# Performance work log

Hardware: AMD Instinct MI355X
Metric: run time of the kernel (lower is better)

The kernel has to match this reference:

```python
import jax, jax.numpy as jnp
import numpy as np

B, T, V, E, H = 4096, 80, 80, 8, 256  # batch, seq_len, num_classes/vocab, embed dim, n_hidden
FORGET_BIAS = 1.0  # tf BasicLSTMCell default


def lstm_layer(x, W, b):
    """Run one BasicLSTMCell layer over time. x: [B, T, D]; W: [D+H, 4H]; b: [4H].
    TF BasicLSTMCell gate order is (i, j, f, o); new_c = c*sig(f+fb) + sig(i)*tanh(j)."""
    Bsz = x.shape[0]

    def step(carry, xt):
        c, h = carry
        gates = jnp.concatenate([xt, h], axis=-1) @ W + b  # [B, 4H]
        i, j, f, o = jnp.split(gates, 4, axis=-1)
        c = c * jax.nn.sigmoid(f + FORGET_BIAS) + jax.nn.sigmoid(i) * jnp.tanh(j)
        h = jnp.tanh(c) * jax.nn.sigmoid(o)
        return (c, h), h

    init = (jnp.zeros((Bsz, H), x.dtype), jnp.zeros((Bsz, H), x.dtype))
    _, hs = jax.lax.scan(step, init, jnp.swapaxes(x, 0, 1))  # hs: [T, B, H]
    return jnp.swapaxes(hs, 0, 1)  # [B, T, H]


def setup_inputs() -> dict:
    key = jax.random.key(0)
    ks = jax.random.split(key, 8)
    features = jax.random.randint(ks[0], (B, T), 0, V, dtype=jnp.int32)
    labels = jax.random.randint(ks[1], (B,), 0, V, dtype=jnp.int32)
    emb = jax.random.normal(ks[2], (V, E), dtype=jnp.float32) * 0.1  # trainable=False in original
    W1 = jax.random.normal(ks[3], (E + H, 4 * H), dtype=jnp.float32) * 0.05
    b1 = jnp.zeros((4 * H,), jnp.float32)
    W2 = jax.random.normal(ks[4], (H + H, 4 * H), dtype=jnp.float32) * 0.05
    b2 = jnp.zeros((4 * H,), jnp.float32)
    Wd = jax.random.normal(ks[5], (H, V), dtype=jnp.float32) * 0.05
    bd = jnp.zeros((V,), jnp.float32)
    return {"features": features, "labels": labels, "emb": emb,
            "W1": W1, "b1": b1, "W2": W2, "b2": b2, "Wd": Wd, "bd": bd}


def reference(features, labels, emb, W1, b1, W2, b2, Wd, bd):
    x = emb[features]                     # [B, T, E] embedding lookup
    h1 = lstm_layer(x, W1, b1)            # [B, T, H]
    h2 = lstm_layer(h1, W2, b2)           # [B, T, H]
    pred = h2[:, -1, :] @ Wd + bd         # [B, V] logits from last timestep
    y = jax.nn.one_hot(labels, V, dtype=pred.dtype)
    loss = jnp.mean(jnp.sum(-y * jax.nn.log_softmax(pred, axis=-1), axis=-1))
    return loss
```

## Files before the change

### kernel.cpp

```cpp
#include <hip/hip_runtime.h>
#include <math.h>

#define B_SZ 4096
#define T_SZ 80
#define V_SZ 80
#define E_SZ 8
#define H_SZ 256
#define G4   1024

typedef __attribute__((ext_vector_type(8))) short short8;
typedef __attribute__((ext_vector_type(4))) float f32x4;

__device__ __forceinline__ float sigm(float x) {
    return 1.f / (1.f + __expf(-x));
}
__device__ __forceinline__ float tanhfast(float x) {
    x = fminf(fmaxf(x, -15.f), 15.f);
    float t = __expf(-2.f * x);
    return (1.f - t) / (1.f + t);
}
__device__ __forceinline__ ushort f2bf(float f) {
    unsigned u = __float_as_uint(f);
    u = (u + 0x7fffu + ((u >> 16) & 1u)) >> 16;
    return (ushort)u;
}

__global__ __launch_bounds__(256) void g1_kernel(const float* __restrict__ emb,
                                                 const float* __restrict__ W1,
                                                 const float* __restrict__ b1,
                                                 float* __restrict__ G1) {
    int idx = blockIdx.x * 256 + threadIdx.x;
    if (idx >= V_SZ * G4) return;
    int v = idx >> 10, col = idx & 1023;
    float g = b1[col];
#pragma unroll
    for (int e = 0; e < E_SZ; e++)
        g += emb[v * E_SZ + e] * W1[e * G4 + col];
    G1[idx] = g;
}

__global__ __launch_bounds__(256) void wtrans(const float* __restrict__ src, int k0,
                                              int Kshift, ushort* __restrict__ out) {
    const int K = 1 << Kshift;
    int idx = blockIdx.x * 256 + threadIdx.x;
    int n = idx >> Kshift, k = idx & (K - 1);
    out[idx] = f2bf(src[(size_t)(k0 + k) * G4 + n]);
}

__global__ __launch_bounds__(256) void wdtrans(const float* __restrict__ src,
                                               ushort* __restrict__ out) {
    int idx = blockIdx.x * 256 + threadIdx.x;
    if (idx >= V_SZ * H_SZ) return;
    int v = idx >> 8, h = idx & 255;
    out[idx] = f2bf(src[h * V_SZ + v]);
}

__global__ __launch_bounds__(256) void lstm_fused(
    const ushort* __restrict__ A1h, int Kend1,
    const int*   __restrict__ feat,
    const float* __restrict__ G1,
    float* __restrict__ c1, ushort* __restrict__ h1out,
    const ushort* __restrict__ A2x, const ushort* __restrict__ A2h, int Kend2,
    const float* __restrict__ b2,
    float* __restrict__ c2, ushort* __restrict__ h2out,
    const ushort* __restrict__ W1t, const ushort* __restrict__ W2t) {

    const int z = blockIdx.z;
    const int Kend = z ? Kend2 : Kend1;
    if (Kend < 0) return;
    const int K = z ? 512 : 256;
    const ushort* __restrict__ Wt = z ? W2t : W1t;

    __shared__ ushort As[128 * 40];
    __shared__ ushort Ws[128 * 40];

    const int tid = threadIdx.x;
    const int w = tid >> 6, l = tid & 63;
    const int l15 = l & 15, l4 = l >> 4;
    const int m0 = blockIdx.x * 128;
    const int h0 = blockIdx.y * 32;

    const int row0 = tid >> 2, c40 = tid & 3;
    const int row1 = row0 + 64;
    const int ncol0 = ((row0) >> 5) * 256 + h0 + (row0 & 31);
    const int ncol1 = ((row1) >> 5) * 256 + h0 + (row1 & 31);
    const size_t wbase0 = (size_t)ncol0 * K + c40 * 8;
    const size_t wbase1 = (size_t)ncol1 * K + c40 * 8;
    const int lA0 = row0 * 40 + c40 * 8, lA1 = row1 * 40 + c40 * 8;

    const int aoff0 = (w * 32 + l15) * 40 + l4 * 8;
    const int aoff1 = aoff0 + 16 * 40;
    const int boff  = l15 * 40 + l4 * 8;

    f32x4 acc[2][8];
    const f32x4 zero4 = {0.f, 0.f, 0.f, 0.f};
#pragma unroll
    for (int fg = 0; fg < 2; fg++)
#pragma unroll
        for (int cf = 0; cf < 8; cf++) acc[fg][cf] = zero4;

    for (int kt = 0; kt < Kend; kt += 32) {
        const ushort* Asrc;
        int kl;
        if (!z)            { Asrc = A1h; kl = kt; }
        else if (kt < 256) { Asrc = A2x; kl = kt; }
        else               { Asrc = A2h; kl = kt - 256; }

        short8 ga0 = *(const short8*)(Asrc + (size_t)(m0 + row0) * H_SZ + kl + c40 * 8);
        short8 ga1 = *(const short8*)(Asrc + (size_t)(m0 + row1) * H_SZ + kl + c40 * 8);
        short8 gw0 = *(const short8*)(Wt + wbase0 + kt);
        short8 gw1 = *(const short8*)(Wt + wbase1 + kt);

        __syncthreads();
        *(short8*)(As + lA0) = ga0;
        *(short8*)(As + lA1) = ga1;
        *(short8*)(Ws + lA0) = gw0;
        *(short8*)(Ws + lA1) = gw1;
        __syncthreads();

        short8 a0 = *(const short8*)(As + aoff0);
        short8 a1 = *(const short8*)(As + aoff1);
#pragma unroll
        for (int cf = 0; cf < 8; cf++) {
            short8 b = *(const short8*)(Ws + boff + cf * 640);
            acc[0][cf] = __builtin_amdgcn_mfma_f32_16x16x32_bf16(a0, b, acc[0][cf], 0, 0, 0);
            acc[1][cf] = __builtin_amdgcn_mfma_f32_16x16x32_bf16(a1, b, acc[1][cf], 0, 0, 0);
        }
    }

    float* __restrict__ cbuf = z ? c2 : c1;
    ushort* __restrict__ hout = z ? h2out : h1out;
    const bool cz = z ? (Kend == 256) : (Kend == 0);

#pragma unroll
    for (int fg = 0; fg < 2; fg++) {
#pragma unroll
        for (int r = 0; r < 4; r++) {
            const int grow = m0 + w * 32 + fg * 16 + l4 * 4 + r;
            const float* gb = z ? b2 : (G1 + (size_t)feat[(size_t)grow * T_SZ] * G4);
#pragma unroll
            for (int h16 = 0; h16 < 2; h16++) {
                const int hcol = h0 + h16 * 16 + l15;
                float gi = acc[fg][0 + h16][r] + gb[hcol];
                float gj = acc[fg][2 + h16][r] + gb[256 + hcol];
                float gf = acc[fg][4 + h16][r] + gb[512 + hcol];
                float go = acc[fg][6 + h16][r] + gb[768 + hcol];
                const size_t ci = (size_t)grow * H_SZ + hcol;
                float cp = cz ? 0.f : cbuf[ci];
                float cn = cp * sigm(gf + 1.f) + sigm(gi) * tanhfast(gj);
                float hn = tanhfast(cn) * sigm(go);
                cbuf[ci] = cn;
                hout[ci] = f2bf(hn);
            }
        }
    }
}

__global__ __launch_bounds__(256) void dense_loss(const ushort* __restrict__ h2,
                                                  const ushort* __restrict__ WdT,
                                                  const float* __restrict__ bd,
                                                  const int* __restrict__ labels,
                                                  float* __restrict__ out) {
    const int tid = threadIdx.x;
    const int w = tid >> 6, l = tid & 63;
    const int l15 = l & 15, l4 = l >> 4;
    const int m0 = blockIdx.x * 64 + w * 16;

    f32x4 acc[5];
    const f32x4 zero4 = {0.f, 0.f, 0.f, 0.f};
#pragma unroll
    for (int cf = 0; cf < 5; cf++) acc[cf] = zero4;

    for (int kt = 0; kt < 256; kt += 32) {
        short8 a = *(const short8*)(h2 + (size_t)(m0 + l15) * H_SZ + l4 * 8 + kt);
#pragma unroll
        for (int cf = 0; cf < 5; cf++) {
            short8 b = *(const short8*)(WdT + (size_t)(cf * 16 + l15) * H_SZ + l4 * 8 + kt);
            acc[cf] = __builtin_amdgcn_mfma_f32_16x16x32_bf16(a, b, acc[cf], 0, 0, 0);
        }
    }
    const float bdv = bd[0 * 16 + l15];
    (void)bdv;
#pragma unroll
    for (int cf = 0; cf < 5; cf++) {
        float bv = bd[cf * 16 + l15];
#pragma unroll
        for (int r = 0; r < 4; r++) acc[cf][r] += bv;
    }

#pragma unroll
    for (int r = 0; r < 4; r++) {
        const int row = m0 + l4 * 4 + r;
        float mx = acc[0][r];
#pragma unroll
        for (int cf = 1; cf < 5; cf++) mx = fmaxf(mx, acc[cf][r]);
#pragma unroll
        for (int msk = 1; msk < 16; msk <<= 1)
            mx = fmaxf(mx, __shfl_xor(mx, msk, 64));
        float s = 0.f;
#pragma unroll
        for (int cf = 0; cf < 5; cf++) s += __expf(acc[cf][r] - mx);
#pragma unroll
        for (int msk = 1; msk < 16; msk <<= 1)
            s += __shfl_xor(s, msk, 64);
        const int lab = labels[row];
        float pl = 0.f;
#pragma unroll
        for (int cf = 0; cf < 5; cf++)
            pl += (cf * 16 + l15 == lab) ? acc[cf][r] : 0.f;
#pragma unroll
        for (int msk = 1; msk < 16; msk <<= 1)
            pl += __shfl_xor(pl, msk, 64);
        if (l15 == 0)
            atomicAdd(out, (logf(s) + mx - pl) * (1.0f / B_SZ));
    }
}

extern "C" void kernel_launch(void* const* d_in, const int* in_sizes, int n_in,
                              void* d_out, int out_size, void* d_ws, size_t ws_size,
                              hipStream_t stream) {
    const int*   features = (const int*)d_in[0];
    const int*   labels   = (const int*)d_in[1];
    const float* emb      = (const float*)d_in[2];
    const float* W1       = (const float*)d_in[3];
    const float* b1       = (const float*)d_in[4];
    const float* W2       = (const float*)d_in[5];
    const float* b2       = (const float*)d_in[6];
    const float* Wd       = (const float*)d_in[7];
    const float* bd       = (const float*)d_in[8];
    float* out = (float*)d_out;

    char* base = (char*)d_ws;
    float*  G1v = (float*)base;                      base += (size_t)V_SZ * G4 * 4;
    float*  c1  = (float*)base;                      base += (size_t)B_SZ * H_SZ * 4;
    float*  c2  = (float*)base;                      base += (size_t)B_SZ * H_SZ * 4;
    ushort* h1b[2]; ushort* h2b[2];
    h1b[0] = (ushort*)base;                          base += (size_t)B_SZ * H_SZ * 2;
    h1b[1] = (ushort*)base;                          base += (size_t)B_SZ * H_SZ * 2;
    h2b[0] = (ushort*)base;                          base += (size_t)B_SZ * H_SZ * 2;
    h2b[1] = (ushort*)base;                          base += (size_t)B_SZ * H_SZ * 2;
    ushort* W1t = (ushort*)base;                     base += (size_t)G4 * H_SZ * 2;
    ushort* W2t = (ushort*)base;                     base += (size_t)G4 * 2 * H_SZ * 2;
    ushort* WdT = (ushort*)base;                     base += (size_t)V_SZ * H_SZ * 2;

    (void)hipMemsetAsync(d_out, 0, sizeof(float), stream);
    g1_kernel<<<(V_SZ * G4 + 255) / 256, 256, 0, stream>>>(emb, W1, b1, G1v);
    wtrans<<<(G4 * 256) / 256, 256, 0, stream>>>(W1, E_SZ, 8, W1t);
    wtrans<<<(G4 * 512) / 256, 256, 0, stream>>>(W2, 0, 9, W2t);
    wdtrans<<<(V_SZ * H_SZ + 255) / 256, 256, 0, stream>>>(Wd, WdT);

    dim3 grid(B_SZ / 128, H_SZ / 32, 2), blk(256);
    for (int t = 0; t <= T_SZ; t++) {
        const int Kend1 = (t < T_SZ) ? (t ? 256 : 0) : -1;
        const int Kend2 = (t >= 1) ? ((t >= 2) ? 512 : 256) : -1;
        lstm_fused<<<grid, blk, 0, stream>>>(
            (t && t < T_SZ) ? h1b[(t - 1) & 1] : nullptr, Kend1,
            features + t, G1v, c1, h1b[t & 1],
            (t >= 1) ? h1b[(t - 1) & 1] : nullptr,
            (t >= 2) ? h2b[(t - 2) & 1] : nullptr, Kend2,
            b2, c2, (t >= 1) ? h2b[(t - 1) & 1] : nullptr,
            W1t, W2t);
    }
    dense_loss<<<B_SZ / 64, 256, 0, stream>>>(h2b[(T_SZ - 1) & 1], WdT, bd, labels, out);
}
```

Baseline: 1.906 ms.

## Double-buffer LDS tiles and prefetch global loads in fused LSTM GEMM

Moves the LSTM step GEMM from a single LDS buffer to two ping-pong buffers. Global loads for tile k+2 are issued while tile k is computed, and tile k+1 is written to the spare buffer, so each iteration needs one barrier instead of two. It also hoists all eight B-fragment LDS reads ahead of the MFMA chain and raises wave priority around the MFMAs. This doubles LDS use per block, which may lower occupancy, and adds register pressure from holding the prefetched values.

```diff
diff --git a/kernel.cpp b/kernel.cpp
--- a/kernel.cpp
+++ b/kernel.cpp
@@ -71,8 +71,8 @@
     const int K = z ? 512 : 256;
     const ushort* __restrict__ Wt = z ? W2t : W1t;
 
-    __shared__ ushort As[128 * 40];
-    __shared__ ushort Ws[128 * 40];
+    __shared__ ushort As[2][128 * 40];
+    __shared__ ushort Ws[2][128 * 40];
 
     const int tid = threadIdx.x;
     const int w = tid >> 6, l = tid & 63;
@@ -82,8 +82,8 @@
 
     const int row0 = tid >> 2, c40 = tid & 3;
     const int row1 = row0 + 64;
-    const int ncol0 = ((row0) >> 5) * 256 + h0 + (row0 & 31);
-    const int ncol1 = ((row1) >> 5) * 256 + h0 + (row1 & 31);
+    const int ncol0 = (row0 >> 5) * 256 + h0 + (row0 & 31);
+    const int ncol1 = (row1 >> 5) * 256 + h0 + (row1 & 31);
     const size_t wbase0 = (size_t)ncol0 * K + c40 * 8;
     const size_t wbase1 = (size_t)ncol1 * K + c40 * 8;
     const int lA0 = row0 * 40 + c40 * 8, lA1 = row1 * 40 + c40 * 8;
@@ -99,33 +99,54 @@
 #pragma unroll
         for (int cf = 0; cf < 8; cf++) acc[fg][cf] = zero4;
 
-    for (int kt = 0; kt < Kend; kt += 32) {
-        const ushort* Asrc;
-        int kl;
+    auto loadTile = [&](int kt, short8& a0, short8& a1, short8& w0, short8& w1) {
+        const ushort* Asrc; int kl;
         if (!z)            { Asrc = A1h; kl = kt; }
         else if (kt < 256) { Asrc = A2x; kl = kt; }
         else               { Asrc = A2h; kl = kt - 256; }
-
-        short8 ga0 = *(const short8*)(Asrc + (size_t)(m0 + row0) * H_SZ + kl + c40 * 8);
-        short8 ga1 = *(const short8*)(Asrc + (size_t)(m0 + row1) * H_SZ + kl + c40 * 8);
-        short8 gw0 = *(const short8*)(Wt + wbase0 + kt);
-        short8 gw1 = *(const short8*)(Wt + wbase1 + kt);
-
+        a0 = *(const short8*)(Asrc + (size_t)(m0 + row0) * H_SZ + kl + c40 * 8);
+        a1 = *(const short8*)(Asrc + (size_t)(m0 + row1) * H_SZ + kl + c40 * 8);
+        w0 = *(const short8*)(Wt + wbase0 + kt);
+        w1 = *(const short8*)(Wt + wbase1 + kt);
+    };
+
+    short8 ga0, ga1, gw0, gw1;
+    if (Kend > 0) {
+        loadTile(0, ga0, ga1, gw0, gw1);
+        *(short8*)(As[0] + lA0) = ga0;
+        *(short8*)(As[0] + lA1) = ga1;
+        *(short8*)(Ws[0] + lA0) = gw0;
+        *(short8*)(Ws[0] + lA1) = gw1;
+        if (Kend > 32) loadTile(32, ga0, ga1, gw0, gw1);
         __syncthreads();
-        *(short8*)(As + lA0) = ga0;
-        *(short8*)(As + lA1) = ga1;
-        *(short8*)(Ws + lA0) = gw0;
-        *(short8*)(Ws + lA1) = gw1;
+    }
+
+    int cur = 0;
+    for (int kt = 0; kt < Kend; kt += 32) {
+        short8 a0 = *(const short8*)(As[cur] + aoff0);
+        short8 a1 = *(const short8*)(As[cur] + aoff1);
+        short8 bq[8];
+#pragma unroll
+        for (int cf = 0; cf < 8; cf++)
+            bq[cf] = *(const short8*)(Ws[cur] + boff + cf * 640);
+
+        __builtin_amdgcn_s_setprio(1);
+#pragma unroll
+        for (int cf = 0; cf < 8; cf++) {
+            acc[0][cf] = __builtin_amdgcn_mfma_f32_16x16x32_bf16(a0, bq[cf], acc[0][cf], 0, 0, 0);
+            acc[1][cf] = __builtin_amdgcn_mfma_f32_16x16x32_bf16(a1, bq[cf], acc[1][cf], 0, 0, 0);
+        }
+        __builtin_amdgcn_s_setprio(0);
+
+        if (kt + 32 < Kend) {
+            *(short8*)(As[cur ^ 1] + lA0) = ga0;
+            *(short8*)(As[cur ^ 1] + lA1) = ga1;
+            *(short8*)(Ws[cur ^ 1] + lA0) = gw0;
+            *(short8*)(Ws[cur ^ 1] + lA1) = gw1;
+            if (kt + 64 < Kend) loadTile(kt + 64, ga0, ga1, gw0, gw1);
+        }
         __syncthreads();
-
-        short8 a0 = *(const short8*)(As + aoff0);
-        short8 a1 = *(const short8*)(As + aoff1);
-#pragma unroll
-        for (int cf = 0; cf < 8; cf++) {
-            short8 b = *(const short8*)(Ws + boff + cf * 640);
-            acc[0][cf] = __builtin_amdgcn_mfma_f32_16x16x32_bf16(a0, b, acc[0][cf], 0, 0, 0);
-            acc[1][cf] = __builtin_amdgcn_mfma_f32_16x16x32_bf16(a1, b, acc[1][cf], 0, 0, 0);
-        }
+        cur ^= 1;
     }
 
     float* __restrict__ cbuf = z ? c2 : c1;
@@ -179,8 +200,6 @@
             acc[cf] = __builtin_amdgcn_mfma_f32_16x16x32_bf16(a, b, acc[cf], 0, 0, 0);
         }
     }
-    const float bdv = bd[0 * 16 + l15];
-    (void)bdv;
 #pragma unroll
     for (int cf = 0; cf < 5; cf++) {
         float bv = bd[cf * 16 + l15];
```

New measurement: 1.589 ms. -16.7%, faster.
